# Kernel optimization log

Measured on AMD Instinct MI355X. Metric: run time of the kernel, lower is better.

Reference implementation:

```python
import jax, jax.numpy as jnp
import numpy as np

B, N, C, D = 1, 8192, 256, 128
MASK_VAL = jnp.float32(-1e16)


def setup_inputs() -> dict:
    key = jax.random.key(0)
    k_in, k_g, k_w, k_b = jax.random.split(key, 4)
    inputs = jax.random.normal(k_in, (B, N, C), dtype=jnp.float32)
    # row has at least one unmasked entry (standard GAT practice).
    graph = (jax.random.uniform(k_g, (N, N)) < 0.01).astype(jnp.float32)
    graph = jnp.maximum(graph, jnp.eye(N, dtype=jnp.float32))
    W = jax.random.normal(k_w, (D, C), dtype=jnp.float32)  # nn.Linear weight [out,in]
    b = jax.random.normal(k_b, (D,), dtype=jnp.float32)
    return {"inputs": inputs, "graph": graph, "W": W, "b": b}


def reference(inputs, graph, W, b):
    # h = W(inputs): [B,N,D]
    h = jnp.einsum('bnc,dc->bnd', inputs, W)
    # dense scores masked by adjacency: [B,N,N]
    scores = jnp.einsum('bnd,bmd->bnm', h, h) * graph[None, :, :]
    # torch: masked_fill_(scores == 0, -1e16)
    scores = jnp.where(scores == 0.0, MASK_VAL, scores)
    attention = jax.nn.softmax(scores, axis=2)
    return jnp.einsum('bnm,bmd->bnd', attention, h) + b
```

## Files before the change

kernel.cpp:

```cpp
#include <hip/hip_runtime.h>
#include <math.h>

#define Nn 8192
#define Cc 256
#define Dd 128
#define CAP 192

typedef float fx4 __attribute__((ext_vector_type(4)));

__global__ __launch_bounds__(256) void wt_kernel(const float* __restrict__ W,
                                                 float4* __restrict__ WT) {
  const int t = blockIdx.x * 256 + threadIdx.x;
  const int c4 = t >> 7;
  const int d  = t & 127;
  const float4 v = *(const float4*)(W + (size_t)d * Cc + c4 * 4);
  WT[c4 * Dd + d] = v;
}

__global__ __launch_bounds__(256) void h_kernel(const float* __restrict__ x,
                                                const float4* __restrict__ WT,
                                                float* __restrict__ h) {
  const int tid = threadIdx.x;
  const int d = tid & 127;
  const int g = tid >> 7;
  const int r0 = blockIdx.x * 16 + g * 8;
  const float4* x4 = (const float4*)(x + (size_t)r0 * Cc);

  float acc[8];
#pragma unroll
  for (int r = 0; r < 8; ++r) acc[r] = 0.f;

#pragma unroll 4
  for (int c4 = 0; c4 < Cc / 4; ++c4) {
    const float4 w = WT[c4 * Dd + d];
#pragma unroll
    for (int r = 0; r < 8; ++r) {
      const float4 u = x4[r * (Cc / 4) + c4];
      acc[r] += u.x * w.x + u.y * w.y + u.z * w.z + u.w * w.w;
    }
  }
#pragma unroll
  for (int r = 0; r < 8; ++r) {
    h[(size_t)(r0 + r) * Dd + d] = acc[r];
  }
}

__global__ __launch_bounds__(256) void scan_kernel(const float* __restrict__ graph,
                                                   int* __restrict__ counts,
                                                   int* __restrict__ edges) {
  __shared__ int idxs[4][CAP];
  const int wv   = threadIdx.x >> 6;
  const int lane = threadIdx.x & 63;
  const int i = blockIdx.x * 4 + wv;
  int* idx = idxs[wv];

  const fx4* row = (const fx4*)(graph + (size_t)i * Nn);
  const unsigned long long lmask = (1ull << lane) - 1ull;
  int cnt = 0;

#pragma unroll
  for (int c = 0; c < 4; ++c) {
    fx4 v[8];
#pragma unroll
    for (int t = 0; t < 8; ++t)
      v[t] = __builtin_nontemporal_load(&row[(c * 8 + t) * 64 + lane]);
#pragma unroll
    for (int t = 0; t < 8; ++t) {
      const int col = 4 * ((c * 8 + t) * 64 + lane);
      {
        const unsigned long long mk = __ballot(v[t].x != 0.f);
        const int p = cnt + __popcll(mk & lmask);
        if (v[t].x != 0.f && p < CAP) idx[p] = col + 0;
        cnt += __popcll(mk);
      }
      {
        const unsigned long long mk = __ballot(v[t].y != 0.f);
        const int p = cnt + __popcll(mk & lmask);
        if (v[t].y != 0.f && p < CAP) idx[p] = col + 1;
        cnt += __popcll(mk);
      }
      {
        const unsigned long long mk = __ballot(v[t].z != 0.f);
        const int p = cnt + __popcll(mk & lmask);
        if (v[t].z != 0.f && p < CAP) idx[p] = col + 2;
        cnt += __popcll(mk);
      }
      {
        const unsigned long long mk = __ballot(v[t].w != 0.f);
        const int p = cnt + __popcll(mk & lmask);
        if (v[t].w != 0.f && p < CAP) idx[p] = col + 3;
        cnt += __popcll(mk);
      }
    }
  }
  const int m = min(cnt, CAP);
  for (int e = lane; e < m; e += 64) edges[(size_t)i * CAP + e] = idx[e];
  if (lane == 0) counts[i] = m;
}

__global__ __launch_bounds__(256) void attn_kernel(const int* __restrict__ counts,
                                                   const int* __restrict__ edges,
                                                   const float* __restrict__ h,
                                                   const float* __restrict__ bias,
                                                   float* __restrict__ out) {
  const int wv   = threadIdx.x >> 6;
  const int lane = threadIdx.x & 63;
  const int i = blockIdx.x * 4 + wv;

  const int m = counts[i];
  const float2 hi2 = *(const float2*)(h + (size_t)i * Dd + lane * 2);
  const int* erow = edges + (size_t)i * CAP;

  float M = -INFINITY, L = 0.f;
  float accx = 0.f, accy = 0.f;

  for (int base = 0; base < m; base += 64) {
    const int nb = min(64, m - base);
    const int jv = (lane < nb) ? erow[base + lane] : i;

    for (int e0 = 0; e0 < nb; e0 += 8) {
      const int ne = min(8, nb - e0);
      float2 hv[8];
#pragma unroll
      for (int t = 0; t < 8; ++t) {
        if (t < ne) {
          const int j = __shfl(jv, e0 + t);
          hv[t] = *(const float2*)(h + (size_t)j * Dd + lane * 2);
        }
      }
#pragma unroll
      for (int t = 0; t < 8; ++t) {
        if (t < ne) {
          float pd = hi2.x * hv[t].x + hi2.y * hv[t].y;
#pragma unroll
          for (int off = 32; off > 0; off >>= 1) pd += __shfl_xor(pd, off);
          const float s = pd;
          if (s != 0.f) {
            const float newM = fmaxf(M, s);
            const float scale = __expf(M - newM);
            const float p = __expf(s - newM);
            L = L * scale + p;
            accx = accx * scale + p * hv[t].x;
            accy = accy * scale + p * hv[t].y;
            M = newM;
          }
        }
      }
    }
  }

  const float inv = 1.f / L;
  const float2 bv = *(const float2*)(bias + lane * 2);
  float2 o;
  o.x = accx * inv + bv.x;
  o.y = accy * inv + bv.y;
  *(float2*)(out + (size_t)i * Dd + lane * 2) = o;
}

extern "C" void kernel_launch(void* const* d_in, const int* in_sizes, int n_in,
                              void* d_out, int out_size, void* d_ws, size_t ws_size,
                              hipStream_t stream) {
  const float* x     = (const float*)d_in[0];
  const float* graph = (const float*)d_in[1];
  const float* W     = (const float*)d_in[2];
  const float* bias  = (const float*)d_in[3];
  float* out = (float*)d_out;

  float*  h      = (float*)d_ws;
  int*    counts = (int*)((char*)d_ws + (size_t)Nn * Dd * 4);
  int*    edges  = counts + Nn;
  float4* WT     = (float4*)((char*)d_ws + (16u << 20));

  wt_kernel<<<32, 256, 0, stream>>>(W, WT);
  h_kernel<<<Nn / 16, 256, 0, stream>>>(x, WT, h);
  scan_kernel<<<Nn / 4, 256, 0, stream>>>(graph, counts, edges);
  attn_kernel<<<Nn / 4, 256, 0, stream>>>(counts, edges, h, bias, out);
}
```

Baseline: 466.9 us.

## Fuse graph scan and attention into one kernel with software-pipelined loads

Merges the adjacency scan and the sparse attention kernels into one, so each wave keeps its row's neighbor list in shared memory instead of writing edges and counts to global memory and reading them back in a second launch. The graph row loads are double-buffered so the next chunk is fetched while the current chunk is ballot-compacted. Neighbor h-row gathers are likewise prefetched one group of eight ahead. This doubles the register footprint for the buffered loads, which may lower occupancy on what is mainly a bandwidth-bound 256 MB graph read.

```diff
diff --git a/kernel.cpp b/kernel.cpp
--- a/kernel.cpp
+++ b/kernel.cpp
@@ -45,25 +45,35 @@
   }
 }
 
-__global__ __launch_bounds__(256) void scan_kernel(const float* __restrict__ graph,
-                                                   int* __restrict__ counts,
-                                                   int* __restrict__ edges) {
+__global__ __launch_bounds__(256) void gat_fused(const float* __restrict__ graph,
+                                                 const float* __restrict__ h,
+                                                 const float* __restrict__ bias,
+                                                 float* __restrict__ out) {
   __shared__ int idxs[4][CAP];
   const int wv   = threadIdx.x >> 6;
   const int lane = threadIdx.x & 63;
   const int i = blockIdx.x * 4 + wv;
   int* idx = idxs[wv];
 
+  const float2 hi2 = *(const float2*)(h + (size_t)i * Dd + lane * 2);
+
   const fx4* row = (const fx4*)(graph + (size_t)i * Nn);
   const unsigned long long lmask = (1ull << lane) - 1ull;
   int cnt = 0;
 
+  fx4 v[8];
+#pragma unroll
+  for (int t = 0; t < 8; ++t)
+    v[t] = __builtin_nontemporal_load(&row[t * 64 + lane]);
+
 #pragma unroll
   for (int c = 0; c < 4; ++c) {
-    fx4 v[8];
+    fx4 nv[8];
+    if (c < 3) {
 #pragma unroll
-    for (int t = 0; t < 8; ++t)
-      v[t] = __builtin_nontemporal_load(&row[(c * 8 + t) * 64 + lane]);
+      for (int t = 0; t < 8; ++t)
+        nv[t] = __builtin_nontemporal_load(&row[(c + 1) * 8 * 64 + t * 64 + lane]);
+    }
 #pragma unroll
     for (int t = 0; t < 8; ++t) {
       const int col = 4 * ((c * 8 + t) * 64 + lane);
@@ -92,61 +102,54 @@
         cnt += __popcll(mk);
       }
     }
+#pragma unroll
+    for (int t = 0; t < 8; ++t) v[t] = nv[t];
   }
   const int m = min(cnt, CAP);
-  for (int e = lane; e < m; e += 64) edges[(size_t)i * CAP + e] = idx[e];
-  if (lane == 0) counts[i] = m;
-}
-
-__global__ __launch_bounds__(256) void attn_kernel(const int* __restrict__ counts,
-                                                   const int* __restrict__ edges,
-                                                   const float* __restrict__ h,
-                                                   const float* __restrict__ bias,
-                                                   float* __restrict__ out) {
-  const int wv   = threadIdx.x >> 6;
-  const int lane = threadIdx.x & 63;
-  const int i = blockIdx.x * 4 + wv;
-
-  const int m = counts[i];
-  const float2 hi2 = *(const float2*)(h + (size_t)i * Dd + lane * 2);
-  const int* erow = edges + (size_t)i * CAP;
 
   float M = -INFINITY, L = 0.f;
   float accx = 0.f, accy = 0.f;
 
-  for (int base = 0; base < m; base += 64) {
-    const int nb = min(64, m - base);
-    const int jv = (lane < nb) ? erow[base + lane] : i;
+  float2 hv[8];
+#pragma unroll
+  for (int t = 0; t < 8; ++t) {
+    if (t < m) {
+      const int j = idx[t];
+      hv[t] = *(const float2*)(h + (size_t)j * Dd + lane * 2);
+    }
+  }
 
-    for (int e0 = 0; e0 < nb; e0 += 8) {
-      const int ne = min(8, nb - e0);
-      float2 hv[8];
+  for (int e0 = 0; e0 < m; e0 += 8) {
+    const int ne = min(8, m - e0);
+    const int rem = m - e0 - 8;
+    float2 nhv[8];
 #pragma unroll
-      for (int t = 0; t < 8; ++t) {
-        if (t < ne) {
-          const int j = __shfl(jv, e0 + t);
-          hv[t] = *(const float2*)(h + (size_t)j * Dd + lane * 2);
-        }
+    for (int t = 0; t < 8; ++t) {
+      if (t < rem) {
+        const int j = idx[e0 + 8 + t];
+        nhv[t] = *(const float2*)(h + (size_t)j * Dd + lane * 2);
       }
+    }
 #pragma unroll
-      for (int t = 0; t < 8; ++t) {
-        if (t < ne) {
-          float pd = hi2.x * hv[t].x + hi2.y * hv[t].y;
+    for (int t = 0; t < 8; ++t) {
+      if (t < ne) {
+        float pd = hi2.x * hv[t].x + hi2.y * hv[t].y;
 #pragma unroll
-          for (int off = 32; off > 0; off >>= 1) pd += __shfl_xor(pd, off);
-          const float s = pd;
-          if (s != 0.f) {
-            const float newM = fmaxf(M, s);
-            const float scale = __expf(M - newM);
-            const float p = __expf(s - newM);
-            L = L * scale + p;
-            accx = accx * scale + p * hv[t].x;
-            accy = accy * scale + p * hv[t].y;
-            M = newM;
-          }
+        for (int off = 32; off > 0; off >>= 1) pd += __shfl_xor(pd, off);
+        const float s = pd;
+        if (s != 0.f) {
+          const float newM = fmaxf(M, s);
+          const float scale = __expf(M - newM);
+          const float p = __expf(s - newM);
+          L = L * scale + p;
+          accx = accx * scale + p * hv[t].x;
+          accy = accy * scale + p * hv[t].y;
+          M = newM;
         }
       }
     }
+#pragma unroll
+    for (int t = 0; t < 8; ++t) hv[t] = nhv[t];
   }
 
   const float inv = 1.f / L;
@@ -166,13 +169,10 @@
   const float* bias  = (const float*)d_in[3];
   float* out = (float*)d_out;
 
-  float*  h      = (float*)d_ws;
-  int*    counts = (int*)((char*)d_ws + (size_t)Nn * Dd * 4);
-  int*    edges  = counts + Nn;
-  float4* WT     = (float4*)((char*)d_ws + (16u << 20));
+  float*  h  = (float*)d_ws;
+  float4* WT = (float4*)((char*)d_ws + (16u << 20));
 
   wt_kernel<<<32, 256, 0, stream>>>(W, WT);
   h_kernel<<<Nn / 16, 256, 0, stream>>>(x, WT, h);
-  scan_kernel<<<Nn / 4, 256, 0, stream>>>(graph, counts, edges);
-  attn_kernel<<<Nn / 4, 256, 0, stream>>>(counts, edges, h, bias, out);
+  gat_fused<<<Nn / 4, 256, 0, stream>>>(graph, h, bias, out);
 }
```

Measured after the change: 459.3 us. About the same (-1.6%).
